# Performance work log

Hardware: AMD Instinct MI355X
Metric: run time of the kernel (lower is better)

## Reference

```python
import jax, jax.numpy as jnp
import numpy as np

NEG = -1e30


def _layernorm(x, g, b, eps=1e-6):
    mu = jnp.mean(x, axis=-1, keepdims=True)
    var = jnp.mean((x - mu) ** 2, axis=-1, keepdims=True)
    return (x - mu) * jax.lax.rsqrt(var + eps) * g + b


def _ctc_loss(log_probs, targets, input_lengths, target_lengths, blank):
    # log_probs: (T, B, V); targets: (B, L) int; lengths: (B,) int
    T, B, V = log_probs.shape
    L = targets.shape[1]
    S = 2 * L + 1
    # extended target sequence: blank, t0, blank, t1, ..., blank
    ext = jnp.full((B, S), blank, dtype=targets.dtype)
    ext = ext.at[:, 1::2].set(targets)
    # skip transition allowed where label differs from label two back and is not blank
    ext_m2 = jnp.pad(ext, ((0, 0), (2, 0)), constant_values=blank)[:, :S]
    skip_mask = (jnp.arange(S)[None, :] >= 2) & (ext != ext_m2) & (ext != blank)
    # gather per-step emission log-probs for extended labels: (T, B, S)
    lp_ext = jnp.take_along_axis(
        log_probs, jnp.broadcast_to(ext[None], (T, B, S)), axis=2
    )

    alpha0 = jnp.full((B, S), NEG, dtype=log_probs.dtype)
    alpha0 = alpha0.at[:, 0].set(lp_ext[0, :, 0])
    alpha0 = alpha0.at[:, 1].set(lp_ext[0, :, 1])

    def step(alpha, lp_e):
        a1 = jnp.pad(alpha, ((0, 0), (1, 0)), constant_values=NEG)[:, :S]
        a2 = jnp.pad(alpha, ((0, 0), (2, 0)), constant_values=NEG)[:, :S]
        a2 = jnp.where(skip_mask, a2, NEG)
        new = jnp.logaddexp(jnp.logaddexp(alpha, a1), a2) + lp_e
        return new, new

    _, alphas_rest = jax.lax.scan(step, alpha0, lp_ext[1:])
    alphas = jnp.concatenate([alpha0[None], alphas_rest], axis=0)  # (T, B, S)

    alpha_T = alphas[input_lengths - 1, jnp.arange(B)]  # (B, S)
    s_end = 2 * target_lengths  # final blank position
    l_blank = jnp.take_along_axis(alpha_T, s_end[:, None], axis=1)[:, 0]
    l_label = jnp.take_along_axis(alpha_T, (s_end - 1)[:, None], axis=1)[:, 0]
    loss_b = -jnp.logaddexp(l_blank, l_label)
    # zero_infinity=True
    loss_b = jnp.where(loss_b > 1e29, 0.0, loss_b)
    # reduction='mean': divide each loss by its target length, then batch-mean
    return jnp.mean(loss_b / target_lengths.astype(loss_b.dtype))


def setup_inputs() -> dict:
    T, B, D, V, L = 2000, 32, 768, 1024, 150
    key = jax.random.key(0)
    ks = jax.random.split(key, 8)
    s = 0.02
    return {
        "source_encoder_output": jax.random.normal(ks[0], (T, B, D), jnp.float32),
        "W_proj": jax.random.normal(ks[1], (D, D), jnp.float32) * s,
        "b_proj": jnp.zeros((D,), jnp.float32),
        "W_tr": jax.random.normal(ks[2], (D, D), jnp.float32) * s,
        "b_tr": jnp.zeros((D,), jnp.float32),
        "ln_g": jnp.ones((D,), jnp.float32),
        "ln_b": jnp.zeros((D,), jnp.float32),
        "W_dec": jax.random.normal(ks[3], (D, V), jnp.float32) * s,
        "b_dec": jnp.zeros((V,), jnp.float32),
        "target_syllabe_ids": jax.random.randint(ks[4], (B, L), 1, V, jnp.int32),
        "source_encoder_output_lengths": jnp.full((B,), T, jnp.int32),
        "target_syllabe_id_lengths": jnp.full((B,), L, jnp.int32),
    }


def reference(source_encoder_output, W_proj, b_proj, W_tr, b_tr, ln_g, ln_b,
              W_dec, b_dec, target_syllabe_ids, source_encoder_output_lengths,
              target_syllabe_id_lengths):
    BLANK = 0
    x = source_encoder_output @ W_proj + b_proj          # encoder_projection
    x = jax.nn.gelu(x @ W_tr + b_tr, approximate=False)  # transform dense + gelu
    x = _layernorm(x, ln_g, ln_b, eps=1e-6)
    scores = x @ W_dec + b_dec                           # acoustic_decoder
    log_probs = jax.nn.log_softmax(scores, axis=-1)      # (T, B, V)
    return _ctc_loss(log_probs, target_syllabe_ids,
                     source_encoder_output_lengths,
                     target_syllabe_id_lengths, BLANK)
```

## Files before the change

### kernel.cpp

```cpp
#include <hip/hip_runtime.h>
#include <hip/hip_bf16.h>
#include <math.h>
#include <stdint.h>

#define NEGF (-1e30f)
#define LOG2E 1.44269504088896340736f
#define LN2 0.69314718055994530942f

#define LPROW 512

typedef short bf16x8 __attribute__((ext_vector_type(8)));
typedef float f32x4 __attribute__((ext_vector_type(4)));
typedef unsigned int u32x4 __attribute__((ext_vector_type(4)));

__device__ __forceinline__ unsigned short f2b(float x) {
  __hip_bfloat16 h = __float2bfloat16(x);
  return *reinterpret_cast<unsigned short*>(&h);
}
__device__ __forceinline__ float b2f(unsigned short u) {
  __hip_bfloat16 h;
  *reinterpret_cast<unsigned short*>(&h) = u;
  return __bfloat162float(h);
}
__device__ __forceinline__ float gelu_exact(float x) {
  return 0.5f * x * (1.0f + erff(x * 0.70710678118654752440f));
}

#if __has_builtin(__builtin_amdgcn_logf)
__device__ __forceinline__ float fast_log2(float x) { return __builtin_amdgcn_logf(x); }
#else
__device__ __forceinline__ float fast_log2(float x) { return log2f(x); }
#endif

template<int CTRL>
__device__ __forceinline__ float dpp_shr(float x) {
  return __int_as_float(__builtin_amdgcn_update_dpp(
      0, __float_as_int(x), 0x110 | CTRL, 0xf, 0xf, true));
}
__device__ __forceinline__ float readlane_f(float x, int l) {
  return __int_as_float(__builtin_amdgcn_readlane(__float_as_int(x), l));
}

__device__ __forceinline__ u32x4 gload_x4(const void* p) {
  u32x4 r;
  asm volatile("global_load_dwordx4 %0, %1, off" : "=v"(r) : "v"(p));
  return r;
}

__device__ __forceinline__ void gload16(void* lds, const void* g) {
  __builtin_amdgcn_global_load_lds(
      (__attribute__((address_space(1))) void*)(uintptr_t)g,
      (__attribute__((address_space(3))) void*)(unsigned int)(uintptr_t)lds,
      16, 0, 0);
}

__global__ __launch_bounds__(256) void cvt_enc_kernel(
    const float* __restrict__ in, unsigned short* __restrict__ out, long n4)
{
  long i = (long)blockIdx.x * blockDim.x + threadIdx.x;
  const long stride = (long)gridDim.x * blockDim.x;
  for (; i < n4; i += stride) {
    float4 v = ((const float4*)in)[i];
    ushort4 o;
    o.x = f2b(v.x); o.y = f2b(v.y); o.z = f2b(v.z); o.w = f2b(v.w);
    ((ushort4*)out)[i] = o;
  }
}

__global__ __launch_bounds__(256) void cvt_wt_kernel(
    const float* __restrict__ W, unsigned short* __restrict__ WT, int K, int N)
{
  __shared__ float tile[32][33];
  const int n0 = blockIdx.x * 32, k0 = blockIdx.y * 32;
  const int tx = threadIdx.x, ty = threadIdx.y;
#pragma unroll
  for (int i = 0; i < 32; i += 8) {
    int k = k0 + ty + i, n = n0 + tx;
    tile[ty + i][tx] = (k < K && n < N) ? W[(long)k * N + n] : 0.f;
  }
  __syncthreads();
#pragma unroll
  for (int i = 0; i < 32; i += 8) {
    int n = n0 + ty + i, k = k0 + tx;
    if (n < N && k < K) WT[(long)n * K + k] = f2b(tile[tx][ty + i]);
  }
}

template<int NFULL, int EPI>
__global__ __launch_bounds__(256, 2) void gemm128_kernel(
    const unsigned short* __restrict__ A,
    const unsigned short* __restrict__ WT,
    const float* __restrict__ bias,
    unsigned short* __restrict__ out,
    float2* __restrict__ partials,
    int K, int gx, int nwg)
{
  extern __shared__ char smem[];
  unsigned short* As = (unsigned short*)smem;
  unsigned short* Bs = (unsigned short*)(smem + 16384);

  const int tid = threadIdx.x, lane = tid & 63, w = tid >> 6;
  const int wr = w >> 1, wc = w & 1;
  const int cl = lane & 15, g = lane >> 4;
  const int bid = blockIdx.x;
  const int wid = (bid & 7) * (nwg >> 3) + (bid >> 3);
  const int bx = wid % gx;
  const long row0 = (long)(wid / gx) * 128;
  const int col0 = bx * 128;

  const int ch0 = w * 64 + lane;
  const int ch1 = 256 + ch0;
  const unsigned short* Ag0 = A + (row0 + (ch0 >> 2)) * K + (ch0 & 3) * 8;
  const unsigned short* Ag1 = A + (row0 + (ch1 >> 2)) * K + (ch1 & 3) * 8;
  const unsigned short* Bg0 = WT + (long)(col0 + (ch0 >> 2)) * K + (ch0 & 3) * 8;
  const unsigned short* Bg1 = WT + (long)(col0 + (ch1 >> 2)) * K + (ch1 & 3) * 8;
  unsigned short* Al0 = As + w * 512;
  unsigned short* Al1 = As + 2048 + w * 512;
  unsigned short* Bl0 = Bs + w * 512;
  unsigned short* Bl1 = Bs + 2048 + w * 512;

#define STAGE(buf, kt)                          \
  do {                                          \
    const int _ko = (kt) * 32;                  \
    gload16(Al0 + (buf) * 4096, Ag0 + _ko);     \
    gload16(Al1 + (buf) * 4096, Ag1 + _ko);     \
    gload16(Bl0 + (buf) * 4096, Bg0 + _ko);     \
    gload16(Bl1 + (buf) * 4096, Bg1 + _ko);     \
  } while (0)

  f32x4 acc[4][4];
#pragma unroll
  for (int mt = 0; mt < 4; ++mt)
#pragma unroll
    for (int nt = 0; nt < 4; ++nt) acc[mt][nt] = (f32x4){0.f, 0.f, 0.f, 0.f};

  const int NKT = K / 32;
  STAGE(0, 0);
  __syncthreads();
  int buf = 0;
  for (int kt = 0; kt < NKT; ++kt) {
    if (kt + 1 < NKT) STAGE(buf ^ 1, kt + 1);
    const unsigned short* Ab = As + buf * 4096;
    const unsigned short* Bb = Bs + buf * 4096;
    bf16x8 af[4], bfr[4];
#pragma unroll
    for (int mt = 0; mt < 4; ++mt)
      af[mt] = *(const bf16x8*)&Ab[(((wr * 64 + mt * 16 + cl) << 2) + g) * 8];
#pragma unroll
    for (int nt = 0; nt < 4; ++nt)
      bfr[nt] = *(const bf16x8*)&Bb[(((wc * 64 + nt * 16 + cl) << 2) + g) * 8];
#pragma unroll
    for (int mt = 0; mt < 4; ++mt)
#pragma unroll
      for (int nt = 0; nt < 4; ++nt)
        acc[mt][nt] = __builtin_amdgcn_mfma_f32_16x16x32_bf16(
            af[mt], bfr[nt], acc[mt][nt], 0, 0, 0);
    __syncthreads();
    buf ^= 1;
  }
#undef STAGE

  float bv[4];
#pragma unroll
  for (int nt = 0; nt < 4; ++nt) bv[nt] = bias[col0 + wc * 64 + nt * 16 + cl];
#pragma unroll
  for (int mt = 0; mt < 4; ++mt)
#pragma unroll
    for (int nt = 0; nt < 4; ++nt)
#pragma unroll
      for (int j = 0; j < 4; ++j) {
        float v = acc[mt][nt][j] + bv[nt];
        if (EPI == 1) v = gelu_exact(v);
        acc[mt][nt][j] = v;
      }

  if (EPI == 2) {
#pragma unroll
    for (int mt = 0; mt < 4; ++mt)
#pragma unroll
      for (int j = 0; j < 4; ++j) {
        float mx = fmaxf(fmaxf(acc[mt][0][j], acc[mt][1][j]),
                         fmaxf(acc[mt][2][j], acc[mt][3][j]));
#pragma unroll
        for (int off = 1; off < 16; off <<= 1)
          mx = fmaxf(mx, __shfl_xor(mx, off));
        float sm = 0.f;
#pragma unroll
        for (int nt = 0; nt < 4; ++nt) sm += expf(acc[mt][nt][j] - mx);
#pragma unroll
        for (int off = 1; off < 16; off <<= 1) sm += __shfl_xor(sm, off);
        if (cl == 0) {
          long m = row0 + wr * 64 + mt * 16 + g * 4 + j;
          partials[m * 16 + bx * 2 + wc] = make_float2(mx, sm);
        }
      }
  }

  unsigned short* Ct = (unsigned short*)smem;
#pragma unroll
  for (int mt = 0; mt < 4; ++mt)
#pragma unroll
    for (int nt = 0; nt < 4; ++nt)
#pragma unroll
      for (int j = 0; j < 4; ++j)
        Ct[(wr * 64 + mt * 16 + g * 4 + j) * 136 + wc * 64 + nt * 16 + cl] =
            f2b(acc[mt][nt][j]);
  __syncthreads();
  for (int idx = tid; idx < 2048; idx += 256) {
    int r = idx >> 4, ch = idx & 15;
    *(bf16x8*)&out[(row0 + r) * NFULL + col0 + ch * 8] =
        *(const bf16x8*)&Ct[r * 136 + ch * 8];
  }
}

template<int D>
__global__ __launch_bounds__(256) void ln_bf16_kernel(
    unsigned short* __restrict__ X, const float* __restrict__ g,
    const float* __restrict__ bt, long M)
{
  constexpr int NI = D / 256;
  const int lane = threadIdx.x & 63;
  const int wid = threadIdx.x >> 6;
  const long row = (long)blockIdx.x * 4 + wid;
  if (row >= M) return;

  float v[NI * 4];
  float s = 0.f;
#pragma unroll
  for (int i = 0; i < NI; ++i) {
    ushort4 u = *(const ushort4*)&X[row * D + (i * 64 + lane) * 4];
    v[i * 4 + 0] = b2f(u.x); v[i * 4 + 1] = b2f(u.y);
    v[i * 4 + 2] = b2f(u.z); v[i * 4 + 3] = b2f(u.w);
    s += v[i * 4 + 0] + v[i * 4 + 1] + v[i * 4 + 2] + v[i * 4 + 3];
  }
#pragma unroll
  for (int off = 32; off; off >>= 1) s += __shfl_xor(s, off);
  const float mu = s * (1.0f / D);
  float q = 0.f;
#pragma unroll
  for (int i = 0; i < NI * 4; ++i) { float d = v[i] - mu; q += d * d; }
#pragma unroll
  for (int off = 32; off; off >>= 1) q += __shfl_xor(q, off);
  const float rs = rsqrtf(q * (1.0f / D) + 1e-6f);
#pragma unroll
  for (int i = 0; i < NI; ++i) {
    ushort4 o;
    int c = (i * 64 + lane) * 4;
    o.x = f2b((v[i * 4 + 0] - mu) * rs * g[c + 0] + bt[c + 0]);
    o.y = f2b((v[i * 4 + 1] - mu) * rs * g[c + 1] + bt[c + 1]);
    o.z = f2b((v[i * 4 + 2] - mu) * rs * g[c + 2] + bt[c + 2]);
    o.w = f2b((v[i * 4 + 3] - mu) * rs * g[c + 3] + bt[c + 3]);
    *(ushort4*)&X[row * D + c] = o;
  }
}

__global__ __launch_bounds__(256) void logz_gather_kernel(
    const unsigned short* __restrict__ scores,
    const float2* __restrict__ partials,
    const int* __restrict__ targets,
    unsigned short* __restrict__ lp_ext,
    long Mtot, int T, int B, int L, int S)
{
  const int w = threadIdx.x >> 6, lane = threadIdx.x & 63;
  const long m = (long)blockIdx.x * 4 + w;
  if (m >= Mtot) return;

  float2 pp = partials[m * 16 + (lane & 15)];
  float Mx = pp.x, Sv = pp.y;
#pragma unroll
  for (int off = 1; off < 16; off <<= 1) {
    float Mo = __shfl_xor(Mx, off);
    float So = __shfl_xor(Sv, off);
    float Mn = fmaxf(Mx, Mo);
    Sv = Sv * expf(Mx - Mn) + So * expf(Mo - Mn);
    Mx = Mn;
  }
  const float logz = Mx + logf(Sv);
  const int b = (int)(m % B);
  const int t = (int)(m / B);
  const unsigned short* srow = scores + m * 1024;
  bf16x8 o = {0, 0, 0, 0, 0, 0, 0, 0};
#pragma unroll
  for (int j = 0; j < 5; ++j) {
    int s = lane * 5 + j;
    if (s < S) {
      int lab = (s & 1) ? targets[b * L + (s >> 1)] : 0;
      o[j] = (short)f2b(expf(b2f(srow[lab]) - logz) * 1024.0f);
    }
  }
  *(bf16x8*)&lp_ext[((long)b * T + t) * LPROW + lane * 8] = o;
}

__global__ __launch_bounds__(64, 1) void ctc_scan_kernel(
    const unsigned short* __restrict__ pr,
    const int* __restrict__ targets, const int* __restrict__ inlens,
    const int* __restrict__ tlens, float* __restrict__ partial,
    int T, int B, int L, int S)
{
  const int b = blockIdx.x;
  const int lane = threadIdx.x;
  const int s0 = lane * 5;
  const int inlen = inlens[b];
  const int tlen = tlens[b];
  const int send = 2 * tlen;
  const int capT = inlen - 1;
  const bool is16 = (lane == 16), is32 = (lane == 32), is48 = (lane == 48);

  const unsigned short* lpb = pr + (long)b * T * LPROW + lane * 8;

  float skm[5];
#pragma unroll
  for (int j = 0; j < 5; ++j) {
    int s = s0 + j;
    float sk = 0.f;
    if (s < S && (s & 1) && s >= 3) {
      int lab = targets[b * L + (s >> 1)];
      int lab2 = targets[b * L + (s >> 1) - 1];
      sk = ((lab != 0) && (lab != lab2)) ? 1.f : 0.f;
    }
    skm[j] = sk;
  }

  float a[5];
  float abv = 0.f, alv = 0.f;
  int corr = 0, corr_cap = 0;
#pragma unroll
  for (int j = 0; j < 5; ++j) {
    int s = s0 + j;
    a[j] = (s <= 1) ? b2f(lpb[j]) : 0.f;
  }
  if (capT == 0) {
#pragma unroll
    for (int j = 0; j < 5; ++j) {
      int s = s0 + j;
      if (s == send) abv = a[j];
      if (s == send - 1) alv = a[j];
    }
    corr_cap = corr;
  }

#define CTC_WAIT                                          \
  do {                                                    \
    asm volatile("s_waitcnt vmcnt(7)" ::: "memory");      \
    __builtin_amdgcn_sched_barrier(0);                    \
  } while (0)

#define CTC_PROCESS(rd, tcur)                                                 \
  do {                                                                        \
    float p0 = __uint_as_float((rd)[0] << 16);                                \
    float p1 = __uint_as_float((rd)[0] & 0xffff0000u);                        \
    float p2 = __uint_as_float((rd)[1] << 16);                                \
    float p3 = __uint_as_float((rd)[1] & 0xffff0000u);                        \
    float p4 = __uint_as_float((rd)[2] << 16);                                \
    float r15 = readlane_f(a[4], 15), r31 = readlane_f(a[4], 31),             \
          r47 = readlane_f(a[4], 47);                                         \
    float q15 = readlane_f(a[3], 15), q31 = readlane_f(a[3], 31),             \
          q47 = readlane_f(a[3], 47);                                         \
    float o_m1 = dpp_shr<1>(a[4]);                                            \
    float o_m2 = dpp_shr<1>(a[3]);                                            \
    o_m1 = is16 ? r15 : o_m1; o_m1 = is32 ? r31 : o_m1;                       \
    o_m1 = is48 ? r47 : o_m1;                                                 \
    o_m2 = is16 ? q15 : o_m2; o_m2 = is32 ? q31 : o_m2;                       \
    o_m2 = is48 ? q47 : o_m2;                                                 \
    float na0 = fmaf(skm[0], o_m2, a[0] + o_m1) * p0;                         \
    float na1 = fmaf(skm[1], o_m1, a[1] + a[0]) * p1;                         \
    float na2 = fmaf(skm[2], a[0], a[2] + a[1]) * p2;                         \
    float na3 = fmaf(skm[3], a[1], a[3] + a[2]) * p3;                         \
    float na4 = fmaf(skm[4], a[2], a[4] + a[3]) * p4;                         \
    a[0] = na0; a[1] = na1; a[2] = na2; a[3] = na3; a[4] = na4;               \
    if ((tcur) == capT) {                                                     \
      _Pragma("unroll")                                                       \
      for (int j = 0; j < 5; ++j) {                                           \
        int s = s0 + j;                                                       \
        if (s == send) abv = a[j];                                            \
        if (s == send - 1) alv = a[j];                                        \
      }                                                                       \
      corr_cap = corr;                                                        \
    }                                                                         \
  } while (0)

#define CTC_RENORM                                                            \
  do {                                                                        \
    float m_ = fmaxf(fmaxf(fmaxf(a[0], a[1]), fmaxf(a[2], a[3])), a[4]);      \
    m_ = fmaxf(m_, dpp_shr<1>(m_));                                           \
    m_ = fmaxf(m_, dpp_shr<2>(m_));                                           \
    m_ = fmaxf(m_, dpp_shr<4>(m_));                                           \
    m_ = fmaxf(m_, dpp_shr<8>(m_));                                           \
    float mx = fmaxf(fmaxf(readlane_f(m_, 15), readlane_f(m_, 31)),           \
                     fmaxf(readlane_f(m_, 47), readlane_f(m_, 63)));          \
    int e;                                                                    \
    (void)frexpf(mx, &e);                      \
    float sc = ldexpf(1.f, -e);                                               \
    _Pragma("unroll")                                                         \
    for (int j = 0; j < 5; ++j) a[j] *= sc;                                   \
    corr += e;                                                                \
  } while (0)

#define CTC_STEP(gN)                                          \
  do {                                                        \
    CTC_WAIT;                                                 \
    if (t < T) CTC_PROCESS(gN, t);                            \
    gN = gload_x4(lpb + (long)(t + 8) * LPROW);               \
    ++t;                                                      \
  } while (0)

  u32x4 g0 = gload_x4(lpb + (long)1 * LPROW);
  u32x4 g1 = gload_x4(lpb + (long)2 * LPROW);
  u32x4 g2 = gload_x4(lpb + (long)3 * LPROW);
  u32x4 g3 = gload_x4(lpb + (long)4 * LPROW);
  u32x4 g4 = gload_x4(lpb + (long)5 * LPROW);
  u32x4 g5 = gload_x4(lpb + (long)6 * LPROW);
  u32x4 g6 = gload_x4(lpb + (long)7 * LPROW);
  u32x4 g7 = gload_x4(lpb + (long)8 * LPROW);

  const int NCH = (T - 1 + 7) / 8;
  int t = 1;
  for (int c = 0; c < NCH; ++c) {
    CTC_STEP(g0);
    CTC_STEP(g1);
    CTC_STEP(g2);
    CTC_STEP(g3);
    CTC_STEP(g4);
    CTC_STEP(g5);
    CTC_STEP(g6);
    CTC_STEP(g7);
    CTC_RENORM;
  }
  asm volatile("s_waitcnt vmcnt(0)" ::: "memory");

#pragma unroll
  for (int off = 32; off; off >>= 1) {
    abv = fmaxf(abv, __shfl_xor(abv, off));
    alv = fmaxf(alv, __shfl_xor(alv, off));
  }
  if (lane == 0) {
    float l2 = fast_log2(abv + alv) + (float)corr_cap - 10.0f * (float)inlen;
    float loss = -LN2 * l2;
    if (!(loss <= 1e29f)) loss = 0.f;
    partial[b] = loss / (float)tlen;
  }
}

__global__ void reduce_kernel(const float* __restrict__ partial,
                              float* __restrict__ out, int B)
{
  int lane = threadIdx.x;
  float v = (lane < B) ? partial[lane] : 0.f;
#pragma unroll
  for (int off = 32; off; off >>= 1) v += __shfl_xor(v, off);
  if (lane == 0) out[0] = v / (float)B;
}

extern "C" void kernel_launch(void* const* d_in, const int* in_sizes, int n_in,
                              void* d_out, int out_size, void* d_ws, size_t ws_size,
                              hipStream_t stream) {
  const float* enc = (const float*)d_in[0];
  const float* Wp  = (const float*)d_in[1];
  const float* bp  = (const float*)d_in[2];
  const float* Wt  = (const float*)d_in[3];
  const float* btr = (const float*)d_in[4];
  const float* lng = (const float*)d_in[5];
  const float* lnb = (const float*)d_in[6];
  const float* Wd  = (const float*)d_in[7];
  const float* bd  = (const float*)d_in[8];
  const int* tgt   = (const int*)d_in[9];
  const int* inl   = (const int*)d_in[10];
  const int* tll   = (const int*)d_in[11];

  const int D = in_sizes[2];
  const int V = in_sizes[8];
  const int B = in_sizes[10];
  const int L = in_sizes[9] / B;
  const long M = (long)in_sizes[0] / D;
  const int T = (int)(M / B);
  const int S = 2 * L + 1;

  char* wsb = (char*)d_ws;
  size_t off = 0;
  auto alloc = [&](size_t bytes) { char* p = wsb + off; off += (bytes + 255) & ~(size_t)255; return p; };
  unsigned short* encb   = (unsigned short*)alloc((size_t)M * D * 2);
  char* x1region         = alloc((size_t)M * V * 2);
  unsigned short* X1b    = (unsigned short*)x1region;
  unsigned short* scores = (unsigned short*)x1region;
  unsigned short* X2b    = encb;
  unsigned short* LP     = (unsigned short*)alloc((size_t)B * T * LPROW * 2 + 65536);
  float2* partials       = (float2*)alloc((size_t)M * 16 * sizeof(float2));
  unsigned short* WpT    = (unsigned short*)alloc((size_t)D * D * 2);
  unsigned short* WtT    = (unsigned short*)alloc((size_t)D * D * 2);
  unsigned short* WdT    = (unsigned short*)alloc((size_t)D * V * 2);
  float* partial         = (float*)alloc(256);

  cvt_wt_kernel<<<dim3(D / 32, D / 32), dim3(32, 8), 0, stream>>>(Wp, WpT, D, D);
  cvt_wt_kernel<<<dim3(D / 32, D / 32), dim3(32, 8), 0, stream>>>(Wt, WtT, D, D);
  cvt_wt_kernel<<<dim3(V / 32, D / 32), dim3(32, 8), 0, stream>>>(Wd, WdT, D, V);
  cvt_enc_kernel<<<2048, 256, 0, stream>>>(enc, encb, (long)M * D / 4);

  const size_t smemg = 34816;
  const int gx12 = D / 128, nwg12 = gx12 * (int)(M / 128);
  const int gx3 = V / 128, nwg3 = gx3 * (int)(M / 128);

  gemm128_kernel<768, 0><<<nwg12, 256, smemg, stream>>>(
      encb, WpT, bp, X1b, nullptr, D, gx12, nwg12);
  gemm128_kernel<768, 1><<<nwg12, 256, smemg, stream>>>(
      X1b, WtT, btr, X2b, nullptr, D, gx12, nwg12);
  ln_bf16_kernel<768><<<(int)(M / 4), 256, 0, stream>>>(X2b, lng, lnb, M);
  gemm128_kernel<1024, 2><<<nwg3, 256, smemg, stream>>>(
      X2b, WdT, bd, scores, partials, D, gx3, nwg3);

  logz_gather_kernel<<<(int)(M / 4), 256, 0, stream>>>(
      scores, partials, tgt, LP, M, T, B, L, S);
  ctc_scan_kernel<<<B, 64, 0, stream>>>(LP, tgt, inl, tll, partial, T, B, L, S);
  reduce_kernel<<<1, 64, 0, stream>>>(partial, (float*)d_out, B);
}
```

Baseline: 762.1 us.

## Fold projection and transform matrices into one combined weight GEMM

Since no nonlinearity sits between the encoder projection and the transform dense layer, the two weight matrices are premultiplied into a single DxD matrix and the biases are folded into bp@Wt+btr. This removes one M x D x D GEMM over the activations, leaving a small DxD GEMM and a bias kernel on the weights. The workspace layout changes (LP now reuses the encoder buffer), and the rounding changes because the combined weight is stored in bf16.

Measured after the change: 875.1 us. 1.15x slower.

```diff
diff --git a/kernel.cpp b/kernel.cpp
--- a/kernel.cpp
+++ b/kernel.cpp
@@ -84,6 +84,17 @@
     int n = n0 + ty + i, k = k0 + tx;
     if (n < N && k < K) WT[(long)n * K + k] = f2b(tile[tx][ty + i]);
   }
+}
+
+__global__ __launch_bounds__(256) void bc_kernel(
+    const float* __restrict__ bp, const float* __restrict__ Wt,
+    const float* __restrict__ btr, float* __restrict__ bc, int D)
+{
+  int n = blockIdx.x * 256 + threadIdx.x;
+  if (n >= D) return;
+  float s = btr[n];
+  for (int k = 0; k < D; ++k) s = fmaf(bp[k], Wt[(long)k * D + n], s);
+  bc[n] = s;
 }
 
 template<int NFULL, int EPI>
@@ -103,7 +114,7 @@
   const int wr = w >> 1, wc = w & 1;
   const int cl = lane & 15, g = lane >> 4;
   const int bid = blockIdx.x;
-  const int wid = (bid & 7) * (nwg >> 3) + (bid >> 3);
+  const int wid = ((nwg & 7) == 0) ? ((bid & 7) * (nwg >> 3) + (bid >> 3)) : bid;
   const int bx = wid % gx;
   const long row0 = (long)(wid / gx) * 128;
   const int col0 = bx * 128;
@@ -389,7 +400,7 @@
     float mx = fmaxf(fmaxf(readlane_f(m_, 15), readlane_f(m_, 31)),           \
                      fmaxf(readlane_f(m_, 47), readlane_f(m_, 63)));          \
     int e;                                                                    \
-    (void)frexpf(mx, &e);                      \
+    (void)frexpf(mx, &e);                                                     \
     float sc = ldexpf(1.f, -e);                                               \
     _Pragma("unroll")                                                         \
     for (int j = 0; j < 5; ++j) a[j] *= sc;                                   \
@@ -479,30 +490,36 @@
   size_t off = 0;
   auto alloc = [&](size_t bytes) { char* p = wsb + off; off += (bytes + 255) & ~(size_t)255; return p; };
   unsigned short* encb   = (unsigned short*)alloc((size_t)M * D * 2);
-  char* x1region         = alloc((size_t)M * V * 2);
-  unsigned short* X1b    = (unsigned short*)x1region;
-  unsigned short* scores = (unsigned short*)x1region;
-  unsigned short* X2b    = encb;
-  unsigned short* LP     = (unsigned short*)alloc((size_t)B * T * LPROW * 2 + 65536);
+  unsigned short* X2b    = (unsigned short*)alloc((size_t)M * D * 2);
+  unsigned short* scores = (unsigned short*)alloc((size_t)M * V * 2);
   float2* partials       = (float2*)alloc((size_t)M * 16 * sizeof(float2));
-  unsigned short* WpT    = (unsigned short*)alloc((size_t)D * D * 2);
   unsigned short* WtT    = (unsigned short*)alloc((size_t)D * D * 2);
+  unsigned short* Wpb    = (unsigned short*)alloc((size_t)D * D * 2);
+  unsigned short* WcT    = (unsigned short*)alloc((size_t)D * D * 2);
   unsigned short* WdT    = (unsigned short*)alloc((size_t)D * V * 2);
+  float* bc              = (float*)alloc((size_t)D * 4);
+  float* zeros           = (float*)alloc((size_t)D * 4);
   float* partial         = (float*)alloc(256);
-
-  cvt_wt_kernel<<<dim3(D / 32, D / 32), dim3(32, 8), 0, stream>>>(Wp, WpT, D, D);
+  unsigned short* LP     = encb;
+
+  hipMemsetAsync(zeros, 0, (size_t)D * 4, stream);
   cvt_wt_kernel<<<dim3(D / 32, D / 32), dim3(32, 8), 0, stream>>>(Wt, WtT, D, D);
+  cvt_enc_kernel<<<256, 256, 0, stream>>>(Wp, Wpb, (long)D * D / 4);
+  {
+    const int gx = D / 128, nwg = gx * (D / 128);
+    gemm128_kernel<768, 0><<<nwg, 256, 34816, stream>>>(
+        WtT, Wpb, zeros, WcT, nullptr, D, gx, nwg);
+  }
+  bc_kernel<<<(D + 255) / 256, 256, 0, stream>>>(bp, Wt, btr, bc, D);
   cvt_wt_kernel<<<dim3(V / 32, D / 32), dim3(32, 8), 0, stream>>>(Wd, WdT, D, V);
   cvt_enc_kernel<<<2048, 256, 0, stream>>>(enc, encb, (long)M * D / 4);
 
   const size_t smemg = 34816;
-  const int gx12 = D / 128, nwg12 = gx12 * (int)(M / 128);
+  const int gx1 = D / 128, nwg1 = gx1 * (int)(M / 128);
   const int gx3 = V / 128, nwg3 = gx3 * (int)(M / 128);
 
-  gemm128_kernel<768, 0><<<nwg12, 256, smemg, stream>>>(
-      encb, WpT, bp, X1b, nullptr, D, gx12, nwg12);
-  gemm128_kernel<768, 1><<<nwg12, 256, smemg, stream>>>(
-      X1b, WtT, btr, X2b, nullptr, D, gx12, nwg12);
+  gemm128_kernel<768, 1><<<nwg1, 256, smemg, stream>>>(
+      encb, WcT, bc, X2b, nullptr, D, gx1, nwg1);
   ln_bf16_kernel<768><<<(int)(M / 4), 256, 0, stream>>>(X2b, lng, lnb, M);
   gemm128_kernel<1024, 2><<<nwg3, 256, smemg, stream>>>(
       X2b, WdT, bd, scores, partials, D, gx3, nwg3);
```
